# Optimization experiments

Hardware: AMD Instinct MI355X
Metric: run time of the kernel (lower is better)

## Reference

```python
import jax, jax.numpy as jnp
import numpy as np

B, T, V, E, H, L = 32, 128, 32000, 512, 512, 3
EPS = 1e-5


def setup_inputs() -> dict:
    key = jax.random.key(0)
    ks = jax.random.split(key, 6)
    idx = jax.random.randint(ks[0], (B, T), 0, V, dtype=jnp.int32)
    emb = jax.random.normal(ks[1], (V, E), dtype=jnp.float32) * 0.02
    # packed gate weights per layer: columns ordered [forget, input, candidate, output]
    # acting on concat([h_prev, x]) of width H+E (matches torch cat order)
    W = jax.random.normal(ks[2], (L, H + E, 4 * H), dtype=jnp.float32) * (1.0 / np.sqrt(H + E))
    b = jnp.zeros((L, 4 * H), dtype=jnp.float32)
    gamma = jnp.ones((H,), dtype=jnp.float32)
    beta = jnp.zeros((H,), dtype=jnp.float32)
    Wh = jax.random.normal(ks[3], (H, V), dtype=jnp.float32) * 0.02
    bh = jnp.zeros((V,), dtype=jnp.float32)
    return {"idx": idx, "emb": emb, "W": W, "b": b, "gamma": gamma, "beta": beta, "Wh": Wh, "bh": bh}


def _lstm_out(idx, emb, W, b):
    x = emb[idx]                       # [B, T, E]
    h0 = jnp.zeros((L, B, H), dtype=x.dtype)
    c0 = jnp.zeros((L, B, H), dtype=x.dtype)

    def step(carry, x_t):
        h, c = carry                   # each [L, B, H]
        new_h, new_c = [], []
        inp = x_t                      # [B, E]
        for i in range(L):
            concat = jnp.concatenate([h[i], inp], axis=1)      # [B, H+E]
            gates = concat @ W[i] + b[i]                       # [B, 4H]
            f, ig, g, o = jnp.split(gates, 4, axis=1)
            f = jax.nn.sigmoid(f)
            ig = jax.nn.sigmoid(ig)
            g = jnp.tanh(g)
            o = jax.nn.sigmoid(o)
            ci = f * c[i] + ig * g
            hi = o * jnp.tanh(ci)
            new_h.append(hi)
            new_c.append(ci)
            inp = hi
        return (jnp.stack(new_h), jnp.stack(new_c)), inp

    _, outs = jax.lax.scan(step, (h0, c0), jnp.swapaxes(x, 0, 1))  # outs: [T, B, H]
    return jnp.swapaxes(outs, 0, 1)    # [B, T, H]


def reference(idx, emb, W, b, gamma, beta, Wh, bh):
    out = _lstm_out(idx, emb, W, b)
    mu = out.mean(-1, keepdims=True)
    var = out.var(-1, keepdims=True)
    out = (out - mu) / jnp.sqrt(var + EPS) * gamma + beta       # LayerNorm
    logits = out @ Wh + bh                                      # [B, T, V]
    return logits
```

## Files before the change

kernel.cpp:

```cpp
#include <hip/hip_runtime.h>

typedef unsigned short u16;
typedef unsigned int u32;
typedef __attribute__((ext_vector_type(8))) __bf16 bf16x8;
typedef __attribute__((ext_vector_type(4))) float f32x4;

#define B_ 32
#define T_ 128
#define V_ 32000
#define H_ 512
#define L_ 3
#define LW 64

__device__ __forceinline__ u16 f2bf(float x) {
  union { float f; u32 u; } v; v.f = x;
  u32 r = v.u + 0x7fffu + ((v.u >> 16) & 1u);
  return (u16)(r >> 16);
}
__device__ __forceinline__ float b2f(u16 h) {
  union { u32 u; float f; } v; v.u = ((u32)h) << 16; return v.f;
}
__device__ __forceinline__ float sigf(float x) { return 1.f / (1.f + __expf(-x)); }
__device__ __forceinline__ float tanhf_(float x) { return 2.f / (1.f + __expf(-2.f * x)) - 1.f; }

__device__ __forceinline__ void gload16(const void* g, void* l) {
  __builtin_amdgcn_global_load_lds((const __attribute__((address_space(1))) u32*)g,
                                   (__attribute__((address_space(3))) u32*)l, 16, 0, 0);
}

union F4B8 { f32x4 f; bf16x8 b; };

__device__ __forceinline__ bf16x8 load_sc1(const void* p) {
  F4B8 r;
  asm volatile("global_load_dwordx4 %0, %1, off sc1" : "=v"(r.f) : "v"(p));
  return r.b;
}
__device__ __forceinline__ void store_short_sc1(void* p, u32 v) {
  asm volatile("global_store_short %0, %1, off sc1" :: "v"(p), "v"(v));
}

__device__ __forceinline__ void wait_epoch(const u32* slots, u32 need, int lane) {
  for (;;) {
    u32 v = __hip_atomic_load(&slots[lane], __ATOMIC_RELAXED, __HIP_MEMORY_SCOPE_AGENT);
    if (__ballot(v >= need) == ~0ull) return;
  }
}

__global__ __launch_bounds__(64) void k_embed(const int* __restrict__ idx,
                                              const float* __restrict__ emb,
                                              u16* __restrict__ X) {
  int bt = blockIdx.x;
  int b = bt >> 7, t = bt & 127;
  int v = idx[bt];
  const float* src = emb + (size_t)v * H_;
  u16* dst = X + ((size_t)t * B_ + b) * H_;
  int l8 = threadIdx.x << 3;
  float4 f0 = *(const float4*)(src + l8);
  float4 f1 = *(const float4*)(src + l8 + 4);
  uint4 o;
  o.x = (u32)f2bf(f0.x) | ((u32)f2bf(f0.y) << 16);
  o.y = (u32)f2bf(f0.z) | ((u32)f2bf(f0.w) << 16);
  o.z = (u32)f2bf(f1.x) | ((u32)f2bf(f1.y) << 16);
  o.w = (u32)f2bf(f1.z) | ((u32)f2bf(f1.w) << 16);
  *(uint4*)(dst + l8) = o;
}

__global__ __launch_bounds__(256) void k_transpose(const float* __restrict__ Wh,
                                                   u16* __restrict__ WhT) {
  __shared__ u16 tile[64][66];
  int nb = blockIdx.x % 500, kb = blockIdx.x / 500;
  int n0 = nb << 6, k0 = kb << 6;
  int tid = threadIdx.x;
#pragma unroll
  for (int it = 0; it < 16; ++it) {
    int k = (it << 2) + (tid >> 6);
    int n = tid & 63;
    tile[k][n] = f2bf(Wh[(size_t)(k0 + k) * V_ + n0 + n]);
  }
  __syncthreads();
#pragma unroll
  for (int it = 0; it < 16; ++it) {
    int n = (it << 2) + (tid >> 6);
    int k = tid & 63;
    WhT[(size_t)(n0 + n) * H_ + k0 + k] = tile[k][n];
  }
}

__global__ __launch_bounds__(128, 1) void k_lstm(const float* __restrict__ Wg,
                                                 const float* __restrict__ bias,
                                                 const u16* __restrict__ X,
                                                 u16* __restrict__ Hbuf,
                                                 u32* __restrict__ done) {
  __shared__ u16 bfrag[32][2][64][8];
  const int l = blockIdx.x / LW, g = blockIdx.x % LW;
  const int tid = threadIdx.x, wave = tid >> 6, lane = tid & 63;

  const float* Wl = Wg + (size_t)l * 1024 * 2048;
  for (int f = tid; f < 4096; f += 128) {
    int kb = f >> 7, nt = (f >> 6) & 1, ln = f & 63;
    int n = (nt << 4) + (ln & 15);
    int col = ((n >> 3) << 9) + (g << 3) + (n & 7);
    int k0 = (kb << 5) + ((ln >> 4) << 3);
#pragma unroll
    for (int j = 0; j < 8; ++j)
      bfrag[kb][nt][ln][j] = f2bf(Wl[(size_t)(k0 + j) * 2048 + col]);
  }
  __syncthreads();
  bf16x8 wfh[16][2], wfx[16][2];
#pragma unroll
  for (int kb = 0; kb < 16; ++kb) {
    wfh[kb][0] = *(const bf16x8*)&bfrag[kb][0][lane][0];
    wfh[kb][1] = *(const bf16x8*)&bfrag[kb][1][lane][0];
    wfx[kb][0] = *(const bf16x8*)&bfrag[16 + kb][0][lane][0];
    wfx[kb][1] = *(const bf16x8*)&bfrag[16 + kb][1][lane][0];
  }

  const int jj = lane & 7, cg = (g << 3) + jj;
  const float bF = bias[l * 2048 + cg];
  const float bI = bias[l * 2048 + 512 + cg];
  const float bG = bias[l * 2048 + 1024 + cg];
  const float bO = bias[l * 2048 + 1536 + cg];
  float cst[4] = {0.f, 0.f, 0.f, 0.f};

  const size_t slice = (size_t)B_ * H_;
  u16* Hl = Hbuf + (size_t)l * (T_ + 1) * slice;
  const u16* inb = (l == 0) ? X : (Hbuf + (size_t)(l - 1) * (T_ + 1) * slice + slice);
  u32* done_own = done + l * 64;
  const u32* done_bel = done + (l > 0 ? (l - 1) * 64 : 0);

  const int mrow = (wave << 4) + (lane & 15);
  const int koff = ((lane >> 4) << 3);

  f32x4 z = {0.f, 0.f, 0.f, 0.f};
  f32x4 pA0 = z, pA1 = z, pB0 = z, pB1 = z;

  auto do_x = [&](int t) {
    const u16* xin = inb + (size_t)t * slice + (size_t)mrow * H_ + koff;
    bf16x8 ax[16];
    if (l == 0) {
#pragma unroll
      for (int kb = 0; kb < 16; ++kb) ax[kb] = *(const bf16x8*)(xin + (kb << 5));
    } else {
#pragma unroll
      for (int kb = 0; kb < 16; ++kb) ax[kb] = load_sc1(xin + (kb << 5));
      asm volatile("s_waitcnt vmcnt(0)" ::: "memory");
      __builtin_amdgcn_sched_barrier(0);
    }
#pragma unroll
    for (int kb = 0; kb < 16; kb += 2) {
      pA0 = __builtin_amdgcn_mfma_f32_16x16x32_bf16(ax[kb], wfx[kb][0], pA0, 0, 0, 0);
      pA1 = __builtin_amdgcn_mfma_f32_16x16x32_bf16(ax[kb], wfx[kb][1], pA1, 0, 0, 0);
      pB0 = __builtin_amdgcn_mfma_f32_16x16x32_bf16(ax[kb + 1], wfx[kb + 1][0], pB0, 0, 0, 0);
      pB1 = __builtin_amdgcn_mfma_f32_16x16x32_bf16(ax[kb + 1], wfx[kb + 1][1], pB1, 0, 0, 0);
    }
  };

  if (l > 0) wait_epoch(done_bel, 1u, lane);
  do_x(0);

  for (int t = 0; t < T_; ++t) {
    if (t > 0) {
      wait_epoch(done_own, (u32)t, lane);
      const u16* hin = Hl + (size_t)t * slice + (size_t)mrow * H_ + koff;
      bf16x8 ah[16];
#pragma unroll
      for (int kb = 0; kb < 16; ++kb) ah[kb] = load_sc1(hin + (kb << 5));
      asm volatile("s_waitcnt vmcnt(0)" ::: "memory");
      __builtin_amdgcn_sched_barrier(0);
#pragma unroll
      for (int kb = 0; kb < 16; kb += 2) {
        pA0 = __builtin_amdgcn_mfma_f32_16x16x32_bf16(ah[kb], wfh[kb][0], pA0, 0, 0, 0);
        pA1 = __builtin_amdgcn_mfma_f32_16x16x32_bf16(ah[kb], wfh[kb][1], pA1, 0, 0, 0);
        pB0 = __builtin_amdgcn_mfma_f32_16x16x32_bf16(ah[kb + 1], wfh[kb + 1][0], pB0, 0, 0, 0);
        pB1 = __builtin_amdgcn_mfma_f32_16x16x32_bf16(ah[kb + 1], wfh[kb + 1][1], pB1, 0, 0, 0);
      }
    }
    {
      f32x4 s0, s1, q0, q1;
#pragma unroll
      for (int r = 0; r < 4; ++r) { s0[r] = pA0[r] + pB0[r]; s1[r] = pA1[r] + pB1[r]; }
#pragma unroll
      for (int r = 0; r < 4; ++r) { q0[r] = __shfl_xor(s0[r], 8); q1[r] = __shfl_xor(s1[r], 8); }
      const bool lo = (lane & 8) == 0;
      float hv[4];
#pragma unroll
      for (int r = 0; r < 4; ++r) {
        float fr = lo ? s0[r] : q0[r];
        float ir = lo ? q0[r] : s0[r];
        float gr = lo ? s1[r] : q1[r];
        float orr = lo ? q1[r] : s1[r];
        float cc = sigf(fr + bF) * cst[r] + sigf(ir + bI) * tanhf_(gr + bG);
        cst[r] = cc;
        hv[r] = sigf(orr + bO) * tanhf_(cc);
      }
      if (lo) {
        int rbase = (wave << 4) + ((lane >> 4) << 2);
        u16* hp = Hl + (size_t)(t + 1) * slice + cg;
#pragma unroll
        for (int r = 0; r < 4; ++r)
          store_short_sc1(hp + (size_t)(rbase + r) * H_, (u32)f2bf(hv[r]));
      }
    }
    asm volatile("s_waitcnt vmcnt(0)" ::: "memory");
    __syncthreads();
    if (tid == 0)
      __hip_atomic_store(&done_own[g], (u32)(t + 1), __ATOMIC_RELAXED, __HIP_MEMORY_SCOPE_AGENT);
    if (t + 1 < T_) {
      pA0 = z; pA1 = z; pB0 = z; pB1 = z;
      if (l > 0) wait_epoch(done_bel, (u32)(t + 2), lane);
      do_x(t + 1);
    }
  }
}

__global__ __launch_bounds__(64) void k_ln(const u16* __restrict__ H2,
                                           const float* __restrict__ gamma,
                                           const float* __restrict__ beta,
                                           u16* __restrict__ Aln) {
  int bt = blockIdx.x;
  int b = bt >> 7, t = bt & 127;
  const u16* src = H2 + ((size_t)(t + 1) * B_ + b) * H_;
  int l8 = threadIdx.x << 3;
  uint4 r = *(const uint4*)(src + l8);
  float v[8];
  v[0] = b2f(r.x & 0xffff); v[1] = b2f(r.x >> 16);
  v[2] = b2f(r.y & 0xffff); v[3] = b2f(r.y >> 16);
  v[4] = b2f(r.z & 0xffff); v[5] = b2f(r.z >> 16);
  v[6] = b2f(r.w & 0xffff); v[7] = b2f(r.w >> 16);
  float s = 0.f, sq = 0.f;
#pragma unroll
  for (int i = 0; i < 8; ++i) { s += v[i]; sq += v[i] * v[i]; }
#pragma unroll
  for (int off = 32; off > 0; off >>= 1) {
    s += __shfl_xor(s, off);
    sq += __shfl_xor(sq, off);
  }
  float mu = s * (1.f / 512.f);
  float inv = rsqrtf(sq * (1.f / 512.f) - mu * mu + 1e-5f);
  float4 g0 = *(const float4*)(gamma + l8), g1 = *(const float4*)(gamma + l8 + 4);
  float4 be0 = *(const float4*)(beta + l8), be1 = *(const float4*)(beta + l8 + 4);
  float gg[8] = {g0.x, g0.y, g0.z, g0.w, g1.x, g1.y, g1.z, g1.w};
  float bb[8] = {be0.x, be0.y, be0.z, be0.w, be1.x, be1.y, be1.z, be1.w};
  u16 o16[8];
#pragma unroll
  for (int i = 0; i < 8; ++i) o16[i] = f2bf((v[i] - mu) * inv * gg[i] + bb[i]);
  uint4 o;
  o.x = (u32)o16[0] | ((u32)o16[1] << 16);
  o.y = (u32)o16[2] | ((u32)o16[3] << 16);
  o.z = (u32)o16[4] | ((u32)o16[5] << 16);
  o.w = (u32)o16[6] | ((u32)o16[7] << 16);
  *(uint4*)(Aln + (size_t)bt * H_ + l8) = o;
}

__global__ __launch_bounds__(256) void k_gemm(const u16* __restrict__ A,
                                              const u16* __restrict__ Bt,
                                              const float* __restrict__ bh,
                                              float* __restrict__ C) {
  __shared__ u16 As[128 * 64], Bs[128 * 64];
  const int bid = blockIdx.x;
  const int mb = bid / 250, nb = bid % 250;
  const size_t arow0 = (size_t)mb << 7;
  const size_t bcol0 = (size_t)nb << 7;
  const int tid = threadIdx.x, wave = tid >> 6, lane = tid & 63;
  const int wm = wave & 1, wn = wave >> 1;
  f32x4 acc[4][4];
  f32x4 z = {0.f, 0.f, 0.f, 0.f};
#pragma unroll
  for (int i = 0; i < 4; ++i)
#pragma unroll
    for (int jj = 0; jj < 4; ++jj) acc[i][jj] = z;

  for (int kt = 0; kt < 8; ++kt) {
#pragma unroll
    for (int it = 0; it < 4; ++it) {
      int rb = (it << 5) + (wave << 3);
      int r = rb + (lane >> 3);
      int kc = ((lane & 7) << 3);
      gload16(A + (arow0 + r) * H_ + (kt << 6) + kc, &As[rb << 6]);
      gload16(Bt + (bcol0 + r) * H_ + (kt << 6) + kc, &Bs[rb << 6]);
    }
    __syncthreads();
#pragma unroll
    for (int kb = 0; kb < 2; ++kb) {
      bf16x8 af[4], bf[4];
#pragma unroll
      for (int mi = 0; mi < 4; ++mi)
        af[mi] = *(const bf16x8*)&As[(((wm << 6) + (mi << 4) + (lane & 15)) << 6) + (kb << 5) + ((lane >> 4) << 3)];
#pragma unroll
      for (int ni = 0; ni < 4; ++ni)
        bf[ni] = *(const bf16x8*)&Bs[(((wn << 6) + (ni << 4) + (lane & 15)) << 6) + (kb << 5) + ((lane >> 4) << 3)];
#pragma unroll
      for (int mi = 0; mi < 4; ++mi)
#pragma unroll
        for (int ni = 0; ni < 4; ++ni)
          acc[mi][ni] = __builtin_amdgcn_mfma_f32_16x16x32_bf16(af[mi], bf[ni], acc[mi][ni], 0, 0, 0);
    }
    __syncthreads();
  }
  const int rb4 = ((lane >> 4) << 2), n0 = lane & 15;
#pragma unroll
  for (int ni = 0; ni < 4; ++ni) {
    size_t col = bcol0 + (wn << 6) + (ni << 4) + n0;
    float bv = bh[col];
#pragma unroll
    for (int mi = 0; mi < 4; ++mi) {
      size_t row = arow0 + (wm << 6) + (mi << 4) + rb4;
#pragma unroll
      for (int r = 0; r < 4; ++r)
        C[(row + r) * V_ + col] = acc[mi][ni][r] + bv;
    }
  }
}

extern "C" void kernel_launch(void* const* d_in, const int* in_sizes, int n_in,
                              void* d_out, int out_size, void* d_ws, size_t ws_size,
                              hipStream_t stream) {
  const int* idx = (const int*)d_in[0];
  const float* emb = (const float*)d_in[1];
  const float* Wg = (const float*)d_in[2];
  const float* bias = (const float*)d_in[3];
  const float* gamma = (const float*)d_in[4];
  const float* beta = (const float*)d_in[5];
  const float* Wh = (const float*)d_in[6];
  const float* bh = (const float*)d_in[7];
  float* out = (float*)d_out;

  char* ws = (char*)d_ws;
  const size_t szX = (size_t)T_ * B_ * H_ * 2;
  const size_t szH = (size_t)L_ * (T_ + 1) * B_ * H_ * 2;
  const size_t szA = (size_t)B_ * T_ * H_ * 2;
  const size_t szW = (size_t)V_ * H_ * 2;
  u16* X = (u16*)ws;
  u16* Hbuf = (u16*)(ws + szX);
  u16* Aln = (u16*)(ws + szX + szH);
  u16* WhT = (u16*)(ws + szX + szH + szA);
  u32* done = (u32*)(ws + szX + szH + szA + szW);
  if (ws_size < szX + szH + szA + szW + (size_t)L_ * 64 * 4) return;

  hipMemsetAsync(done, 0, L_ * 64 * 4, stream);
  k_embed<<<B_ * T_, 64, 0, stream>>>(idx, emb, X);
  k_transpose<<<500 * 8, 256, 0, stream>>>(Wh, WhT);
  k_lstm<<<L_ * LW, 128, 0, stream>>>(Wg, bias, X, Hbuf, done);
  k_ln<<<B_ * T_, 64, 0, stream>>>(Hbuf + (size_t)2 * (T_ + 1) * B_ * H_, gamma, beta, Aln);
  k_gemm<<<32 * 250, 256, 0, stream>>>(Aln, WhT, bh, out);
}
```

Before: 894.4 us.

## Replace epoch-flag handshakes with NaN-sentinel polling on hidden-state buffers

The hidden-state buffers are pre-filled with 0xFF, which reads as bf16 NaN. Each consumer now reloads its h or x tile and recomputes the MFMA until the accumulators hold no NaN, instead of waiting on per-group epoch counters. This drops the per-step vmcnt drain, the __syncthreads, the atomic flag store and the ballot spin on flag slots, so data arrival itself acts as the signal. The x and h contributions now go into separate accumulators. In exchange there is a ~12 MB memset per call, repeated loads and MFMAs while spinning, and reliance on NaN propagation and on the order in which other blocks' stores become visible, with no explicit fence. It would also hang if a genuine inf or NaN appeared in the data.

```diff
diff --git a/kernel.cpp b/kernel.cpp
--- a/kernel.cpp
+++ b/kernel.cpp
@@ -39,11 +39,10 @@
   asm volatile("global_store_short %0, %1, off sc1" :: "v"(p), "v"(v));
 }
 
-__device__ __forceinline__ void wait_epoch(const u32* slots, u32 need, int lane) {
-  for (;;) {
-    u32 v = __hip_atomic_load(&slots[lane], __ATOMIC_RELAXED, __HIP_MEMORY_SCOPE_AGENT);
-    if (__ballot(v >= need) == ~0ull) return;
-  }
+__device__ __forceinline__ bool acc_nan(const f32x4& a, const f32x4& b) {
+  float s = a[0] + a[1] + a[2] + a[3] + b[0] + b[1] + b[2] + b[3];
+  union { float f; u32 u; } v; v.f = s;
+  return __ballot(v.u + v.u > 0xFF000000u) != 0ull;
 }
 
 __global__ __launch_bounds__(64) void k_embed(const int* __restrict__ idx,
@@ -89,8 +88,7 @@
 __global__ __launch_bounds__(128, 1) void k_lstm(const float* __restrict__ Wg,
                                                  const float* __restrict__ bias,
                                                  const u16* __restrict__ X,
-                                                 u16* __restrict__ Hbuf,
-                                                 u32* __restrict__ done) {
+                                                 u16* __restrict__ Hbuf) {
   __shared__ u16 bfrag[32][2][64][8];
   const int l = blockIdx.x / LW, g = blockIdx.x % LW;
   const int tid = threadIdx.x, wave = tid >> 6, lane = tid & 63;
@@ -125,60 +123,77 @@
   const size_t slice = (size_t)B_ * H_;
   u16* Hl = Hbuf + (size_t)l * (T_ + 1) * slice;
   const u16* inb = (l == 0) ? X : (Hbuf + (size_t)(l - 1) * (T_ + 1) * slice + slice);
-  u32* done_own = done + l * 64;
-  const u32* done_bel = done + (l > 0 ? (l - 1) * 64 : 0);
 
   const int mrow = (wave << 4) + (lane & 15);
   const int koff = ((lane >> 4) << 3);
 
   f32x4 z = {0.f, 0.f, 0.f, 0.f};
-  f32x4 pA0 = z, pA1 = z, pB0 = z, pB1 = z;
+  f32x4 pxA0 = z, pxA1 = z, pxB0 = z, pxB1 = z;
 
   auto do_x = [&](int t) {
     const u16* xin = inb + (size_t)t * slice + (size_t)mrow * H_ + koff;
-    bf16x8 ax[16];
     if (l == 0) {
+      bf16x8 ax[16];
 #pragma unroll
       for (int kb = 0; kb < 16; ++kb) ax[kb] = *(const bf16x8*)(xin + (kb << 5));
+      pxA0 = z; pxA1 = z; pxB0 = z; pxB1 = z;
+#pragma unroll
+      for (int kb = 0; kb < 16; kb += 2) {
+        pxA0 = __builtin_amdgcn_mfma_f32_16x16x32_bf16(ax[kb], wfx[kb][0], pxA0, 0, 0, 0);
+        pxA1 = __builtin_amdgcn_mfma_f32_16x16x32_bf16(ax[kb], wfx[kb][1], pxA1, 0, 0, 0);
+        pxB0 = __builtin_amdgcn_mfma_f32_16x16x32_bf16(ax[kb + 1], wfx[kb + 1][0], pxB0, 0, 0, 0);
+        pxB1 = __builtin_amdgcn_mfma_f32_16x16x32_bf16(ax[kb + 1], wfx[kb + 1][1], pxB1, 0, 0, 0);
+      }
     } else {
-#pragma unroll
-      for (int kb = 0; kb < 16; ++kb) ax[kb] = load_sc1(xin + (kb << 5));
-      asm volatile("s_waitcnt vmcnt(0)" ::: "memory");
-      __builtin_amdgcn_sched_barrier(0);
-    }
-#pragma unroll
-    for (int kb = 0; kb < 16; kb += 2) {
-      pA0 = __builtin_amdgcn_mfma_f32_16x16x32_bf16(ax[kb], wfx[kb][0], pA0, 0, 0, 0);
-      pA1 = __builtin_amdgcn_mfma_f32_16x16x32_bf16(ax[kb], wfx[kb][1], pA1, 0, 0, 0);
-      pB0 = __builtin_amdgcn_mfma_f32_16x16x32_bf16(ax[kb + 1], wfx[kb + 1][0], pB0, 0, 0, 0);
-      pB1 = __builtin_amdgcn_mfma_f32_16x16x32_bf16(ax[kb + 1], wfx[kb + 1][1], pB1, 0, 0, 0);
+      for (;;) {
+        bf16x8 ax[16];
+#pragma unroll
+        for (int kb = 0; kb < 16; ++kb) ax[kb] = load_sc1(xin + (kb << 5));
+        asm volatile("s_waitcnt vmcnt(0)" ::: "memory");
+        __builtin_amdgcn_sched_barrier(0);
+        pxA0 = z; pxA1 = z; pxB0 = z; pxB1 = z;
+#pragma unroll
+        for (int kb = 0; kb < 16; kb += 2) {
+          pxA0 = __builtin_amdgcn_mfma_f32_16x16x32_bf16(ax[kb], wfx[kb][0], pxA0, 0, 0, 0);
+          pxA1 = __builtin_amdgcn_mfma_f32_16x16x32_bf16(ax[kb], wfx[kb][1], pxA1, 0, 0, 0);
+          pxB0 = __builtin_amdgcn_mfma_f32_16x16x32_bf16(ax[kb + 1], wfx[kb + 1][0], pxB0, 0, 0, 0);
+          pxB1 = __builtin_amdgcn_mfma_f32_16x16x32_bf16(ax[kb + 1], wfx[kb + 1][1], pxB1, 0, 0, 0);
+        }
+        if (!acc_nan(pxA0, pxB0)) break;
+      }
     }
   };
 
-  if (l > 0) wait_epoch(done_bel, 1u, lane);
   do_x(0);
 
   for (int t = 0; t < T_; ++t) {
+    f32x4 hA0 = z, hA1 = z, hB0 = z, hB1 = z;
     if (t > 0) {
-      wait_epoch(done_own, (u32)t, lane);
       const u16* hin = Hl + (size_t)t * slice + (size_t)mrow * H_ + koff;
-      bf16x8 ah[16];
-#pragma unroll
-      for (int kb = 0; kb < 16; ++kb) ah[kb] = load_sc1(hin + (kb << 5));
-      asm volatile("s_waitcnt vmcnt(0)" ::: "memory");
-      __builtin_amdgcn_sched_barrier(0);
-#pragma unroll
-      for (int kb = 0; kb < 16; kb += 2) {
-        pA0 = __builtin_amdgcn_mfma_f32_16x16x32_bf16(ah[kb], wfh[kb][0], pA0, 0, 0, 0);
-        pA1 = __builtin_amdgcn_mfma_f32_16x16x32_bf16(ah[kb], wfh[kb][1], pA1, 0, 0, 0);
-        pB0 = __builtin_amdgcn_mfma_f32_16x16x32_bf16(ah[kb + 1], wfh[kb + 1][0], pB0, 0, 0, 0);
-        pB1 = __builtin_amdgcn_mfma_f32_16x16x32_bf16(ah[kb + 1], wfh[kb + 1][1], pB1, 0, 0, 0);
+      for (;;) {
+        bf16x8 ah[16];
+#pragma unroll
+        for (int kb = 0; kb < 16; ++kb) ah[kb] = load_sc1(hin + (kb << 5));
+        asm volatile("s_waitcnt vmcnt(0)" ::: "memory");
+        __builtin_amdgcn_sched_barrier(0);
+        hA0 = z; hA1 = z; hB0 = z; hB1 = z;
+#pragma unroll
+        for (int kb = 0; kb < 16; kb += 2) {
+          hA0 = __builtin_amdgcn_mfma_f32_16x16x32_bf16(ah[kb], wfh[kb][0], hA0, 0, 0, 0);
+          hA1 = __builtin_amdgcn_mfma_f32_16x16x32_bf16(ah[kb], wfh[kb][1], hA1, 0, 0, 0);
+          hB0 = __builtin_amdgcn_mfma_f32_16x16x32_bf16(ah[kb + 1], wfh[kb + 1][0], hB0, 0, 0, 0);
+          hB1 = __builtin_amdgcn_mfma_f32_16x16x32_bf16(ah[kb + 1], wfh[kb + 1][1], hB1, 0, 0, 0);
+        }
+        if (!acc_nan(hA0, hB0)) break;
       }
     }
     {
       f32x4 s0, s1, q0, q1;
 #pragma unroll
-      for (int r = 0; r < 4; ++r) { s0[r] = pA0[r] + pB0[r]; s1[r] = pA1[r] + pB1[r]; }
+      for (int r = 0; r < 4; ++r) {
+        s0[r] = pxA0[r] + pxB0[r] + hA0[r] + hB0[r];
+        s1[r] = pxA1[r] + pxB1[r] + hA1[r] + hB1[r];
+      }
 #pragma unroll
       for (int r = 0; r < 4; ++r) { q0[r] = __shfl_xor(s0[r], 8); q1[r] = __shfl_xor(s1[r], 8); }
       const bool lo = (lane & 8) == 0;
@@ -201,15 +216,7 @@
           store_short_sc1(hp + (size_t)(rbase + r) * H_, (u32)f2bf(hv[r]));
       }
     }
-    asm volatile("s_waitcnt vmcnt(0)" ::: "memory");
-    __syncthreads();
-    if (tid == 0)
-      __hip_atomic_store(&done_own[g], (u32)(t + 1), __ATOMIC_RELAXED, __HIP_MEMORY_SCOPE_AGENT);
-    if (t + 1 < T_) {
-      pA0 = z; pA1 = z; pB0 = z; pB1 = z;
-      if (l > 0) wait_epoch(done_bel, (u32)(t + 2), lane);
-      do_x(t + 1);
-    }
+    if (t + 1 < T_) do_x(t + 1);
   }
 }
 
@@ -334,13 +341,15 @@
   u16* Hbuf = (u16*)(ws + szX);
   u16* Aln = (u16*)(ws + szX + szH);
   u16* WhT = (u16*)(ws + szX + szH + szA);
-  u32* done = (u32*)(ws + szX + szH + szA + szW);
-  if (ws_size < szX + szH + szA + szW + (size_t)L_ * 64 * 4) return;
-
-  hipMemsetAsync(done, 0, L_ * 64 * 4, stream);
+  if (ws_size < szX + szH + szA + szW) return;
+
+  const size_t slice = (size_t)B_ * H_;
+  hipMemsetAsync(Hbuf, 0xFF, szH, stream);
+  for (int l = 0; l < L_; ++l)
+    hipMemsetAsync(Hbuf + (size_t)l * (T_ + 1) * slice, 0, slice * 2, stream);
   k_embed<<<B_ * T_, 64, 0, stream>>>(idx, emb, X);
   k_transpose<<<500 * 8, 256, 0, stream>>>(Wh, WhT);
-  k_lstm<<<L_ * LW, 128, 0, stream>>>(Wg, bias, X, Hbuf, done);
+  k_lstm<<<L_ * LW, 128, 0, stream>>>(Wg, bias, X, Hbuf);
   k_ln<<<B_ * T_, 64, 0, stream>>>(Hbuf + (size_t)2 * (T_ + 1) * B_ * H_, gamma, beta, Aln);
   k_gemm<<<32 * 250, 256, 0, stream>>>(Aln, WhT, bh, out);
 }
```

Result: slower. 1.124 ms (+25.7%).
